# Kernel tuning notes

Measured on AMD Instinct MI355X. Metric: run time of the kernel, lower is better.

Reference implementation:

```python
import jax, jax.numpy as jnp
import numpy as np

EMBED_DIM = 1024
NUM_HEADS = 16
HEAD_DIM = EMBED_DIM // NUM_HEADS
SCALE = HEAD_DIM ** -0.5


def setup_inputs() -> dict:
    key = jax.random.key(0)
    k1, k2, k3, k4 = jax.random.split(key, 4)
    B, N, D = 2, 2048, EMBED_DIM
    x = jax.random.normal(k1, (B, N, D), dtype=jnp.float32)
    # nn.Linear weights stored as [out, in]; we keep [in, out] for x @ W
    w_qkv = jax.random.normal(k2, (D, 3 * D), dtype=jnp.float32) * (D ** -0.5)
    w_proj = jax.random.normal(k3, (D, D), dtype=jnp.float32) * (D ** -0.5)
    b_proj = jax.random.normal(k4, (D,), dtype=jnp.float32) * 0.01
    return {"x": x, "w_qkv": w_qkv, "w_proj": w_proj, "b_proj": b_proj}


def reference(x, w_qkv, w_proj, b_proj):
    B, N, D = x.shape
    H, Hd = NUM_HEADS, HEAD_DIM
    qkv = x @ w_qkv  # [B, N, 3D]
    q, k, v = jnp.split(qkv, 3, axis=-1)
    # [B, N, D] -> [B, H, N, Hd]
    split_heads = lambda t: t.reshape(B, N, H, Hd).transpose(0, 2, 1, 3)
    q, k, v = split_heads(q), split_heads(k), split_heads(v)
    a = jnp.einsum("bhqd,bhkd->bhqk", q, k) * SCALE
    a = jax.nn.softmax(a, axis=-1)
    out = jnp.einsum("bhqk,bhkd->bhqd", a, v)
    out = out.transpose(0, 2, 1, 3).reshape(B, N, D)
    return out @ w_proj + b_proj
```

## Files before the change

### kernel.cpp

```cpp
#include <hip/hip_runtime.h>
#include <stdint.h>

typedef __attribute__((ext_vector_type(8))) short bf16x8;
typedef __attribute__((ext_vector_type(4))) float f32x4;
typedef __attribute__((ext_vector_type(4))) float float4v;
typedef __attribute__((ext_vector_type(8))) unsigned short u16x8;

#define DEV __device__ __forceinline__

DEV unsigned short f2bf(float f) {
    union { float f; uint32_t u; } v; v.f = f;
    uint32_t u = v.u;
    return (unsigned short)((u + 0x7FFFu + ((u >> 16) & 1u)) >> 16);
}

DEV unsigned int cvt_pk_bf16(float lo, float hi) {
    unsigned int r;
    asm("v_cvt_pk_bf16_f32 %0, %1, %2" : "=v"(r) : "v"(lo), "v"(hi));
    return r;
}

#if __has_builtin(__builtin_amdgcn_global_load_lds)
#define HAVE_GLDS 1
typedef const unsigned char __attribute__((address_space(1)))* as1p;
typedef unsigned char __attribute__((address_space(3)))* as3p;
DEV void gload16(const unsigned short* g, unsigned short* l) {
    __builtin_amdgcn_global_load_lds((as1p)(const void*)g, (as3p)(void*)l, 16, 0, 0);
}
#else
#define HAVE_GLDS 0
#endif

__global__ void k_cvt_x(const float* __restrict__ x, unsigned short* __restrict__ xb, int n4) {
    int i = blockIdx.x * blockDim.x + threadIdx.x;
    if (i >= n4) return;
    float4v v = *(const float4v*)(x + (size_t)i * 4);
    union { unsigned short s[4]; uint64_t q; } o;
    o.s[0] = f2bf(v[0]); o.s[1] = f2bf(v[1]); o.s[2] = f2bf(v[2]); o.s[3] = f2bf(v[3]);
    *(uint64_t*)(xb + (size_t)i * 4) = o.q;
}

__global__ void k_cvt_tr_w(const float* __restrict__ w, unsigned short* __restrict__ wt,
                           int R, int C) {
    __shared__ alignas(16) unsigned short tile[64][65];
    const int t = threadIdx.x;
    const int tr = blockIdx.y * 64, tc = blockIdx.x * 64;
#pragma unroll
    for (int p = 0; p < 4; ++p) {
        int r = p * 16 + (t >> 4);
        int c = (t & 15) * 4;
        float4v v = *(const float4v*)(w + (size_t)(tr + r) * C + tc + c);
#pragma unroll
        for (int j = 0; j < 4; ++j) tile[r][c + j] = f2bf(v[j]);
    }
    __syncthreads();
#pragma unroll
    for (int p = 0; p < 2; ++p) {
        int r2 = p * 32 + (t >> 3);
        int k0 = (t & 7) * 8;
        u16x8 o;
#pragma unroll
        for (int j = 0; j < 8; ++j) o[j] = tile[k0 + j][r2];
        *(u16x8*)(wt + (size_t)(tc + r2) * R + tr + k0) = o;
    }
}

template <int OUT_BF16>
__global__ __launch_bounds__(256)
void k_gemm_bt(const unsigned short* __restrict__ A,
               const unsigned short* __restrict__ Bt,
               void* __restrict__ Cp, const float* __restrict__ bias,
               int M, int N, int K) {
    __shared__ alignas(16) unsigned short lA[128 * 64];
    __shared__ alignas(16) unsigned short lB[128 * 64];
    const int t = threadIdx.x;
    const int w = t >> 6, l = t & 63;
    const int l15 = l & 15, l4 = l >> 4;
    const int wm = (w >> 1) * 64, wn = (w & 1) * 64;
    const size_t bm = (size_t)blockIdx.y * 128, bn = (size_t)blockIdx.x * 128;

    int offA[4][2], offB[4][2];
#pragma unroll
    for (int f = 0; f < 4; ++f) {
        const int ra = wm + f * 16 + l15;
        const int rb = wn + f * 16 + l15;
#pragma unroll
        for (int kc = 0; kc < 2; ++kc) {
            offA[f][kc] = ra * 64 + (((kc * 4 + l4) ^ (ra & 7)) << 3);
            offB[f][kc] = rb * 64 + (((kc * 4 + l4) ^ (rb & 7)) << 3);
        }
    }

#if HAVE_GLDS
    const int srow8 = l >> 3;
    const int scol  = (l & 7) ^ srow8;
    const unsigned short* gA = A  + (bm + w * 32 + srow8) * (size_t)K + scol * 8;
    const unsigned short* gB = Bt + (bn + w * 32 + srow8) * (size_t)K + scol * 8;
    unsigned short* dA = lA + (w * 32) * 64;
    unsigned short* dB = lB + (w * 32) * 64;
#else
    const int srow = t >> 3, sslot = t & 7;
    const int swoff = srow * 64 + ((sslot ^ (srow & 7)) << 3);
    const unsigned short* pA = A + (bm + srow) * (size_t)K + sslot * 8;
    const unsigned short* pB = Bt + (bn + srow) * (size_t)K + sslot * 8;
#endif

    const f32x4 zf = {0.f, 0.f, 0.f, 0.f};
    f32x4 acc[4][4];
#pragma unroll
    for (int i = 0; i < 4; ++i)
#pragma unroll
        for (int j = 0; j < 4; ++j) acc[i][j] = zf;

    for (int kt = 0; kt < K; kt += 64) {
#if HAVE_GLDS
        __syncthreads();
#pragma unroll
        for (int i = 0; i < 4; ++i) {
            gload16(gA + (size_t)i * 8 * K + kt, dA + i * 8 * 64);
            gload16(gB + (size_t)i * 8 * K + kt, dB + i * 8 * 64);
        }
        __syncthreads();
#else
        bf16x8 ra[4], rb[4];
#pragma unroll
        for (int p = 0; p < 4; ++p) {
            ra[p] = *(const bf16x8*)(pA + (size_t)p * 32 * K + kt);
            rb[p] = *(const bf16x8*)(pB + (size_t)p * 32 * K + kt);
        }
        __syncthreads();
#pragma unroll
        for (int p = 0; p < 4; ++p) {
            *(bf16x8*)(lA + p * 32 * 64 + swoff) = ra[p];
            *(bf16x8*)(lB + p * 32 * 64 + swoff) = rb[p];
        }
        __syncthreads();
#endif
#pragma unroll
        for (int kc = 0; kc < 2; ++kc) {
            bf16x8 af[4], bfr[4];
#pragma unroll
            for (int f = 0; f < 4; ++f) af[f] = *(const bf16x8*)(lA + offA[f][kc]);
#pragma unroll
            for (int f = 0; f < 4; ++f) bfr[f] = *(const bf16x8*)(lB + offB[f][kc]);
#pragma unroll
            for (int mf = 0; mf < 4; ++mf)
#pragma unroll
                for (int nf = 0; nf < 4; ++nf)
                    acc[mf][nf] = __builtin_amdgcn_mfma_f32_16x16x32_bf16(
                        af[mf], bfr[nf], acc[mf][nf], 0, 0, 0);
        }
    }

    if (OUT_BF16) {
        unsigned short* C = (unsigned short*)Cp;
#pragma unroll
        for (int mf = 0; mf < 4; ++mf)
#pragma unroll
            for (int nf = 0; nf < 4; ++nf) {
                const size_t row = bm + wm + mf * 16 + l4 * 4;
                const size_t col = bn + wn + nf * 16 + l15;
#pragma unroll
                for (int j = 0; j < 4; ++j)
                    C[(row + j) * (size_t)N + col] = f2bf(acc[mf][nf][j]);
            }
    } else {
        float* C = (float*)Cp;
#pragma unroll
        for (int nf = 0; nf < 4; ++nf) {
            const size_t col = bn + wn + nf * 16 + l15;
            const float bv = bias[col];
#pragma unroll
            for (int mf = 0; mf < 4; ++mf) {
                const size_t row = bm + wm + mf * 16 + l4 * 4;
#pragma unroll
                for (int j = 0; j < 4; ++j)
                    C[(row + j) * (size_t)N + col] = acc[mf][nf][j] + bv;
            }
        }
    }
}

__global__ void k_tr_v(const unsigned short* __restrict__ qkv, unsigned short* __restrict__ vt) {
    __shared__ alignas(16) unsigned short tile[64][72];
    const int t = threadIdx.x;
    const int bh = blockIdx.y, b = bh >> 4, h = bh & 15;
    const int nb = blockIdx.x * 64;
#pragma unroll
    for (int p = 0; p < 2; ++p) {
        const int n = p * 32 + (t >> 3), d0 = (t & 7) * 8;
        u16x8 v = *(const u16x8*)(qkv + (size_t)(b * 2048 + nb + n) * 3072 + 2048 + h * 64 + d0);
#pragma unroll
        for (int j = 0; j < 8; ++j) tile[d0 + j][n] = v[j];
    }
    __syncthreads();
#pragma unroll
    for (int p = 0; p < 2; ++p) {
        const int d = p * 32 + (t >> 3), n0 = (t & 7) * 8;
        u16x8 v = *(const u16x8*)(&tile[d][n0]);
        *(u16x8*)(vt + (size_t)(bh * 64 + d) * 2048 + nb + n0) = v;
    }
}

__global__ __launch_bounds__(256, 4)
void k_attn(const unsigned short* __restrict__ qkv, const unsigned short* __restrict__ vt,
            unsigned short* __restrict__ attn_out) {
    __shared__ alignas(16) unsigned short lK[2][64 * 64];
    __shared__ alignas(16) unsigned short lV[2][64 * 64];
    __shared__ alignas(16) unsigned short lP[4][16 * 64];
    const int t = threadIdx.x, w = t >> 6, l = t & 63;
    const int l15 = l & 15, l4 = l >> 4;
    const int bh = blockIdx.y, b = bh >> 4, h = bh & 15;
    const int qb = blockIdx.x * 64;
    const float QSCALE = 0.18033688011112042f;

    const unsigned short* qptr =
        qkv + (size_t)(b * 2048 + qb + w * 16 + l15) * 3072 + h * 64 + l4 * 8;
    const bf16x8 aq0 = *(const bf16x8*)(qptr);
    const bf16x8 aq1 = *(const bf16x8*)(qptr + 32);

    const int srow = t >> 3, sslot = t & 7;
    const int swoff = srow * 64 + ((sslot ^ (srow & 7)) << 3);
    const unsigned short* kptr = qkv + (size_t)(b * 2048 + srow) * 3072 + 1024 + h * 64 + sslot * 8;
    const unsigned short* vptr = vt + (size_t)(bh * 64 + srow) * 2048 + sslot * 8;

    int offK[4][2];
#pragma unroll
    for (int nf = 0; nf < 4; ++nf) {
        const int r = nf * 16 + l15;
#pragma unroll
        for (int kc = 0; kc < 2; ++kc)
            offK[nf][kc] = r * 64 + (((kc * 4 + l4) ^ (r & 7)) << 3);
    }
    int offPw[4];
#pragma unroll
    for (int nf = 0; nf < 4; ++nf) {
        const int c = nf * 16 + l4 * 4;
        offPw[nf] = l15 * 64 + (((c >> 3) ^ (l15 & 7)) << 3) + (c & 7);
    }

    const f32x4 zf = {0.f, 0.f, 0.f, 0.f};
    f32x4 o[4];
#pragma unroll
    for (int df = 0; df < 4; ++df) o[df] = zf;
    f32x4 accl = zf;
    float m_run = -1e30f;
    unsigned short* Pw = &lP[w][0];
    const bf16x8 ones8 = {(short)0x3F80, (short)0x3F80, (short)0x3F80, (short)0x3F80,
                          (short)0x3F80, (short)0x3F80, (short)0x3F80, (short)0x3F80};

    {
        bf16x8 rk[2], rv[2];
#pragma unroll
        for (int p = 0; p < 2; ++p) {
            rk[p] = *(const bf16x8*)(kptr + (size_t)(p * 32) * 3072);
            rv[p] = *(const bf16x8*)(vptr + (size_t)(p * 32) * 2048);
        }
#pragma unroll
        for (int p = 0; p < 2; ++p) {
            *(bf16x8*)(&lK[0][0] + p * 32 * 64 + swoff) = rk[p];
            *(bf16x8*)(&lV[0][0] + p * 32 * 64 + swoff) = rv[p];
        }
        __syncthreads();
    }

#pragma unroll 2
    for (int kt = 0; kt < 2048; kt += 64) {
        const int cur = (kt >> 6) & 1;
        const unsigned short* K = &lK[cur][0];
        const unsigned short* V = &lV[cur][0];

        bf16x8 rk[2], rv[2];
        const bool more = (kt + 64) < 2048;
        if (more) {
#pragma unroll
            for (int p = 0; p < 2; ++p) {
                rk[p] = *(const bf16x8*)(kptr + (size_t)(kt + 64 + p * 32) * 3072);
                rv[p] = *(const bf16x8*)(vptr + (size_t)(p * 32) * 2048 + kt + 64);
            }
        }

        f32x4 s[4];
        __builtin_amdgcn_s_setprio(1);
#pragma unroll
        for (int nf = 0; nf < 4; ++nf) {
            const bf16x8 kf0 = *(const bf16x8*)(K + offK[nf][0]);
            const bf16x8 kf1 = *(const bf16x8*)(K + offK[nf][1]);
            f32x4 a = zf;
            a = __builtin_amdgcn_mfma_f32_16x16x32_bf16(kf0, aq0, a, 0, 0, 0);
            a = __builtin_amdgcn_mfma_f32_16x16x32_bf16(kf1, aq1, a, 0, 0, 0);
            s[nf] = a;
        }
        __builtin_amdgcn_s_setprio(0);

        float mx = fmaxf(fmaxf(s[0][0], s[0][1]), s[0][2]);
        mx = fmaxf(fmaxf(mx, s[0][3]), s[1][0]);
        mx = fmaxf(fmaxf(mx, s[1][1]), s[1][2]);
        mx = fmaxf(fmaxf(mx, s[1][3]), s[2][0]);
        mx = fmaxf(fmaxf(mx, s[2][1]), s[2][2]);
        mx = fmaxf(fmaxf(mx, s[2][3]), s[3][0]);
        mx = fmaxf(fmaxf(mx, s[3][1]), s[3][2]);
        mx = fmaxf(mx, s[3][3]);
        mx = fmaxf(mx, __shfl_xor(mx, 16));
        mx = fmaxf(mx, __shfl_xor(mx, 32));
        mx *= QSCALE;

        if (!__all(mx <= m_run + 8.0f)) {
            const float mn = fmaxf(m_run, mx);
            const float alpha = exp2f(m_run - mn);
            m_run = mn;
            const float a0 = __shfl(alpha, l4 * 4 + 0);
            const float a1 = __shfl(alpha, l4 * 4 + 1);
            const float a2 = __shfl(alpha, l4 * 4 + 2);
            const float a3 = __shfl(alpha, l4 * 4 + 3);
#pragma unroll
            for (int df = 0; df < 4; ++df) {
                o[df][0] *= a0; o[df][1] *= a1; o[df][2] *= a2; o[df][3] *= a3;
            }
            accl[0] *= a0; accl[1] *= a1; accl[2] *= a2; accl[3] *= a3;
        }

#pragma unroll
        for (int nf = 0; nf < 4; ++nf) {
            const float p0 = exp2f(fmaf(s[nf][0], QSCALE, -m_run));
            const float p1 = exp2f(fmaf(s[nf][1], QSCALE, -m_run));
            const float p2 = exp2f(fmaf(s[nf][2], QSCALE, -m_run));
            const float p3 = exp2f(fmaf(s[nf][3], QSCALE, -m_run));
            union { unsigned int d[2]; uint64_t q; } u;
            u.d[0] = cvt_pk_bf16(p0, p1);
            u.d[1] = cvt_pk_bf16(p2, p3);
            *(uint64_t*)(Pw + offPw[nf]) = u.q;
        }

        const bf16x8 ap0 = *(const bf16x8*)(Pw + l15 * 64 + ((l4 ^ (l15 & 7)) << 3));
        const bf16x8 ap1 = *(const bf16x8*)(Pw + l15 * 64 + (((4 + l4) ^ (l15 & 7)) << 3));
        __builtin_amdgcn_s_setprio(1);
        accl = __builtin_amdgcn_mfma_f32_16x16x32_bf16(ap0, ones8, accl, 0, 0, 0);
        accl = __builtin_amdgcn_mfma_f32_16x16x32_bf16(ap1, ones8, accl, 0, 0, 0);
#pragma unroll
        for (int df = 0; df < 4; ++df) {
            const int r = df * 16 + l15;
            const bf16x8 bv0 = *(const bf16x8*)(V + r * 64 + ((l4 ^ (r & 7)) << 3));
            const bf16x8 bv1 = *(const bf16x8*)(V + r * 64 + (((4 + l4) ^ (r & 7)) << 3));
            o[df] = __builtin_amdgcn_mfma_f32_16x16x32_bf16(ap0, bv0, o[df], 0, 0, 0);
            o[df] = __builtin_amdgcn_mfma_f32_16x16x32_bf16(ap1, bv1, o[df], 0, 0, 0);
        }
        __builtin_amdgcn_s_setprio(0);

        if (more) {
#pragma unroll
            for (int p = 0; p < 2; ++p) {
                *(bf16x8*)(&lK[cur ^ 1][0] + p * 32 * 64 + swoff) = rk[p];
                *(bf16x8*)(&lV[cur ^ 1][0] + p * 32 * 64 + swoff) = rv[p];
            }
        }
        __syncthreads();
    }

    const float r0 = 1.0f / accl[0];
    const float r1 = 1.0f / accl[1];
    const float r2 = 1.0f / accl[2];
    const float r3 = 1.0f / accl[3];
    const int rowb = b * 2048 + qb + w * 16 + l4 * 4;
#pragma unroll
    for (int df = 0; df < 4; ++df) {
        const int d = df * 16 + l15;
        attn_out[(size_t)(rowb + 0) * 1024 + h * 64 + d] = f2bf(o[df][0] * r0);
        attn_out[(size_t)(rowb + 1) * 1024 + h * 64 + d] = f2bf(o[df][1] * r1);
        attn_out[(size_t)(rowb + 2) * 1024 + h * 64 + d] = f2bf(o[df][2] * r2);
        attn_out[(size_t)(rowb + 3) * 1024 + h * 64 + d] = f2bf(o[df][3] * r3);
    }
}

extern "C" void kernel_launch(void* const* d_in, const int* in_sizes, int n_in,
                              void* d_out, int out_size, void* d_ws, size_t ws_size,
                              hipStream_t stream) {
    const float* x      = (const float*)d_in[0];
    const float* w_qkv  = (const float*)d_in[1];
    const float* w_proj = (const float*)d_in[2];
    const float* b_proj = (const float*)d_in[3];
    float* out = (float*)d_out;

    char* ws = (char*)d_ws;
    unsigned short* xb     = (unsigned short*)(ws + 0);
    unsigned short* wqkvT  = (unsigned short*)(ws + 8388608);
    unsigned short* wprojT = (unsigned short*)(ws + 14680064);
    unsigned short* qkv    = (unsigned short*)(ws + 16777216);
    unsigned short* vt     = (unsigned short*)(ws + 41943040);
    unsigned short* attn   = (unsigned short*)(ws + 50331648);

    k_cvt_x<<<dim3(4096), dim3(256), 0, stream>>>(x, xb, 4096 * 1024 / 4);
    k_cvt_tr_w<<<dim3(48, 16), dim3(256), 0, stream>>>(w_qkv, wqkvT, 1024, 3072);
    k_cvt_tr_w<<<dim3(16, 16), dim3(256), 0, stream>>>(w_proj, wprojT, 1024, 1024);
    k_gemm_bt<1><<<dim3(24, 32), dim3(256), 0, stream>>>(xb, wqkvT, (void*)qkv, (const float*)nullptr, 4096, 3072, 1024);
    k_tr_v<<<dim3(32, 32), dim3(256), 0, stream>>>(qkv, vt);
    k_attn<<<dim3(32, 32), dim3(256), 0, stream>>>(qkv, vt, attn);
    k_gemm_bt<0><<<dim3(8, 32), dim3(256), 0, stream>>>(attn, wprojT, (void*)out, b_proj, 4096, 1024, 1024);
}
```

Baseline: 141.1 us.

## Fuse V transpose into QKV GEMM epilogue and async-load K/V tiles to LDS

The QKV GEMM epilogue now writes V columns straight into the transposed vt layout, so the separate k_tr_v kernel and its extra pass over V are gone. Separately, when global_load_lds is available, the attention kernel streams K and V tiles into LDS with direct global-to-LDS loads that apply the XOR swizzle through the source addressing. This drops the register staging and the explicit LDS stores. The cost is scattered 8-byte stores in the GEMM epilogue and a dependence on the async load path's ordering with __syncthreads.

```diff
diff --git a/kernel.cpp b/kernel.cpp
--- a/kernel.cpp
+++ b/kernel.cpp
@@ -70,6 +70,7 @@
 void k_gemm_bt(const unsigned short* __restrict__ A,
                const unsigned short* __restrict__ Bt,
                void* __restrict__ Cp, const float* __restrict__ bias,
+               unsigned short* __restrict__ vt_out,
                int M, int N, int K) {
     __shared__ alignas(16) unsigned short lA[128 * 64];
     __shared__ alignas(16) unsigned short lB[128 * 64];
@@ -153,17 +154,34 @@
     }
 
     if (OUT_BF16) {
-        unsigned short* C = (unsigned short*)Cp;
-#pragma unroll
-        for (int mf = 0; mf < 4; ++mf)
+        if (vt_out && bn >= 2048) {
+            const int bb = (int)(bm >> 11);
+            const int n0 = (int)(bm & 2047) + wm + l4 * 4;
 #pragma unroll
             for (int nf = 0; nf < 4; ++nf) {
-                const size_t row = bm + wm + mf * 16 + l4 * 4;
-                const size_t col = bn + wn + nf * 16 + l15;
-#pragma unroll
-                for (int j = 0; j < 4; ++j)
-                    C[(row + j) * (size_t)N + col] = f2bf(acc[mf][nf][j]);
-            }
+                const int d = (int)(bn - 2048) + wn + nf * 16 + l15;
+                unsigned short* vrow = vt_out + ((size_t)(bb * 16 + (d >> 6)) * 64 + (d & 63)) * 2048;
+#pragma unroll
+                for (int mf = 0; mf < 4; ++mf) {
+                    union { unsigned short s[4]; uint64_t q; } u;
+#pragma unroll
+                    for (int j = 0; j < 4; ++j) u.s[j] = f2bf(acc[mf][nf][j]);
+                    *(uint64_t*)(vrow + n0 + mf * 16) = u.q;
+                }
+            }
+        } else {
+            unsigned short* C = (unsigned short*)Cp;
+#pragma unroll
+            for (int mf = 0; mf < 4; ++mf)
+#pragma unroll
+                for (int nf = 0; nf < 4; ++nf) {
+                    const size_t row = bm + wm + mf * 16 + l4 * 4;
+                    const size_t col = bn + wn + nf * 16 + l15;
+#pragma unroll
+                    for (int j = 0; j < 4; ++j)
+                        C[(row + j) * (size_t)N + col] = f2bf(acc[mf][nf][j]);
+                }
+        }
     } else {
         float* C = (float*)Cp;
 #pragma unroll
@@ -178,27 +196,6 @@
                     C[(row + j) * (size_t)N + col] = acc[mf][nf][j] + bv;
             }
         }
-    }
-}
-
-__global__ void k_tr_v(const unsigned short* __restrict__ qkv, unsigned short* __restrict__ vt) {
-    __shared__ alignas(16) unsigned short tile[64][72];
-    const int t = threadIdx.x;
-    const int bh = blockIdx.y, b = bh >> 4, h = bh & 15;
-    const int nb = blockIdx.x * 64;
-#pragma unroll
-    for (int p = 0; p < 2; ++p) {
-        const int n = p * 32 + (t >> 3), d0 = (t & 7) * 8;
-        u16x8 v = *(const u16x8*)(qkv + (size_t)(b * 2048 + nb + n) * 3072 + 2048 + h * 64 + d0);
-#pragma unroll
-        for (int j = 0; j < 8; ++j) tile[d0 + j][n] = v[j];
-    }
-    __syncthreads();
-#pragma unroll
-    for (int p = 0; p < 2; ++p) {
-        const int d = p * 32 + (t >> 3), n0 = (t & 7) * 8;
-        u16x8 v = *(const u16x8*)(&tile[d][n0]);
-        *(u16x8*)(vt + (size_t)(bh * 64 + d) * 2048 + nb + n0) = v;
     }
 }
 
@@ -219,10 +216,17 @@
     const bf16x8 aq0 = *(const bf16x8*)(qptr);
     const bf16x8 aq1 = *(const bf16x8*)(qptr + 32);
 
+#if HAVE_GLDS
+    const int gr = l >> 3;
+    const int gs = (l & 7) ^ gr;
+    const unsigned short* gK = qkv + (size_t)(b * 2048 + w * 16 + gr) * 3072 + 1024 + h * 64 + gs * 8;
+    const unsigned short* gV = vt + (size_t)(bh * 64 + w * 16 + gr) * 2048 + gs * 8;
+#else
     const int srow = t >> 3, sslot = t & 7;
     const int swoff = srow * 64 + ((sslot ^ (srow & 7)) << 3);
     const unsigned short* kptr = qkv + (size_t)(b * 2048 + srow) * 3072 + 1024 + h * 64 + sslot * 8;
     const unsigned short* vptr = vt + (size_t)(bh * 64 + srow) * 2048 + sslot * 8;
+#endif
 
     int offK[4][2];
 #pragma unroll
@@ -249,6 +253,14 @@
     const bf16x8 ones8 = {(short)0x3F80, (short)0x3F80, (short)0x3F80, (short)0x3F80,
                           (short)0x3F80, (short)0x3F80, (short)0x3F80, (short)0x3F80};
 
+#if HAVE_GLDS
+#pragma unroll
+    for (int i = 0; i < 2; ++i) {
+        gload16(gK + (size_t)i * 8 * 3072, &lK[0][(w * 16 + i * 8) * 64]);
+        gload16(gV + (size_t)i * 8 * 2048, &lV[0][(w * 16 + i * 8) * 64]);
+    }
+    __syncthreads();
+#else
     {
         bf16x8 rk[2], rv[2];
 #pragma unroll
@@ -263,15 +275,25 @@
         }
         __syncthreads();
     }
+#endif
 
 #pragma unroll 2
     for (int kt = 0; kt < 2048; kt += 64) {
         const int cur = (kt >> 6) & 1;
         const unsigned short* K = &lK[cur][0];
         const unsigned short* V = &lV[cur][0];
-
+        const bool more = (kt + 64) < 2048;
+
+#if HAVE_GLDS
+        if (more) {
+#pragma unroll
+            for (int i = 0; i < 2; ++i) {
+                gload16(gK + (size_t)(kt + 64 + i * 8) * 3072, &lK[cur ^ 1][(w * 16 + i * 8) * 64]);
+                gload16(gV + (size_t)i * 8 * 2048 + kt + 64,   &lV[cur ^ 1][(w * 16 + i * 8) * 64]);
+            }
+        }
+#else
         bf16x8 rk[2], rv[2];
-        const bool more = (kt + 64) < 2048;
         if (more) {
 #pragma unroll
             for (int p = 0; p < 2; ++p) {
@@ -279,6 +301,7 @@
                 rv[p] = *(const bf16x8*)(vptr + (size_t)(p * 32) * 2048 + kt + 64);
             }
         }
+#endif
 
         f32x4 s[4];
         __builtin_amdgcn_s_setprio(1);
@@ -347,6 +370,7 @@
         }
         __builtin_amdgcn_s_setprio(0);
 
+#if !HAVE_GLDS
         if (more) {
 #pragma unroll
             for (int p = 0; p < 2; ++p) {
@@ -354,6 +378,7 @@
                 *(bf16x8*)(&lV[cur ^ 1][0] + p * 32 * 64 + swoff) = rv[p];
             }
         }
+#endif
         __syncthreads();
     }
 
@@ -392,8 +417,7 @@
     k_cvt_x<<<dim3(4096), dim3(256), 0, stream>>>(x, xb, 4096 * 1024 / 4);
     k_cvt_tr_w<<<dim3(48, 16), dim3(256), 0, stream>>>(w_qkv, wqkvT, 1024, 3072);
     k_cvt_tr_w<<<dim3(16, 16), dim3(256), 0, stream>>>(w_proj, wprojT, 1024, 1024);
-    k_gemm_bt<1><<<dim3(24, 32), dim3(256), 0, stream>>>(xb, wqkvT, (void*)qkv, (const float*)nullptr, 4096, 3072, 1024);
-    k_tr_v<<<dim3(32, 32), dim3(256), 0, stream>>>(qkv, vt);
+    k_gemm_bt<1><<<dim3(24, 32), dim3(256), 0, stream>>>(xb, wqkvT, (void*)qkv, (const float*)nullptr, vt, 4096, 3072, 1024);
     k_attn<<<dim3(32, 32), dim3(256), 0, stream>>>(qkv, vt, attn);
-    k_gemm_bt<0><<<dim3(8, 32), dim3(256), 0, stream>>>(attn, wprojT, (void*)out, b_proj, 4096, 1024, 1024);
-}
+    k_gemm_bt<0><<<dim3(8, 32), dim3(256), 0, stream>>>(attn, wprojT, (void*)out, b_proj, (unsigned short*)nullptr, 4096, 1024, 1024);
+}
```

New measurement: 139.1 us. About the same (-1.4%).
